# Kernel optimization log

Measured on AMD Instinct MI355X. Metric: run time of the kernel, lower is better.

Reference implementation:

```python
import jax, jax.numpy as jnp
import numpy as np

N_ENT = 14951   # entities (FB15K-style multimodal KG)
N_REL = 1345    # relations == number of context sub-graphs
N_NODES = 120000  # nodes in the batched context graph (b_x length)
N_EDGES = 480000  # edges in the normalized batched adjacency


def _glorot(key, shape):
    scale = np.sqrt(2.0 / (shape[0] + shape[1])).astype(np.float32)
    return jax.random.normal(key, shape, dtype=jnp.float32) * scale


def setup_inputs() -> dict:
    key = jax.random.key(0)
    ks = jax.random.split(key, 16)
    inp = {}
    inp["img_feat"] = jax.random.normal(ks[0], (N_ENT, 4096), dtype=jnp.float32)
    inp["text_feat"] = jax.random.normal(ks[1], (N_ENT, 300), dtype=jnp.float32)
    inp["rel_emb"] = jax.random.normal(ks[2], (N_REL, 300), dtype=jnp.float32)
    # learned parameters (eval mode: dropout = identity)
    inp["W_img_text"] = _glorot(ks[3], (4396, 100)); inp["b_img_text"] = jnp.zeros((100,), jnp.float32)
    inp["W_rel_input"] = _glorot(ks[4], (300, 100)); inp["b_rel_input"] = jnp.zeros((100,), jnp.float32)
    inp["W_gc1"] = _glorot(ks[5], (200, 256)); inp["b_gc1"] = jnp.zeros((256,), jnp.float32)
    inp["W_gc2"] = _glorot(ks[6], (256, 200)); inp["b_gc2"] = jnp.zeros((200,), jnp.float32)
    inp["W_emb"] = _glorot(ks[7], (400, 1)); inp["b_emb"] = jnp.zeros((1,), jnp.float32)
    inp["W_emb_out"] = _glorot(ks[8], (400, 200)); inp["b_emb_out"] = jnp.zeros((200,), jnp.float32)
    inp["W_rel"] = _glorot(ks[9], (300, 200)); inp["b_rel"] = jnp.zeros((200,), jnp.float32)
    # row-normalized adjacency of the batched context graph, as edge list
    inp["edge_weight"] = jax.random.uniform(ks[10], (N_EDGES,), dtype=jnp.float32)
    inp["b_x"] = jax.random.randint(ks[11], (N_NODES,), 0, N_ENT)
    inp["b_graph"] = jax.random.randint(ks[12], (N_NODES,), 0, N_REL)
    inp["edge_src"] = jax.random.randint(ks[13], (N_EDGES,), 0, N_NODES)
    inp["edge_dst"] = jax.random.randint(ks[14], (N_EDGES,), 0, N_NODES)
    return inp


def reference(img_feat, text_feat, rel_emb, W_img_text, b_img_text, W_rel_input,
              b_rel_input, W_gc1, b_gc1, W_gc2, b_gc2, W_emb, b_emb, W_emb_out,
              b_emb_out, W_rel, b_rel, edge_weight, b_x, b_graph, edge_src, edge_dst):
    seg_sum = lambda v, idx, n: jax.ops.segment_sum(v, idx, num_segments=n)

    def spmm(h):  # normalized adjacency @ h via edge-list gather/scatter
        return seg_sum(h[edge_src] * edge_weight[:, None], edge_dst, N_NODES)

    # multimodal entity encoder: Linear(4396 -> 100)
    emf = jnp.concatenate([img_feat, text_feat], axis=1) @ W_img_text + b_img_text
    # relation context encoder: Linear(300 -> 100) + ReLU
    rel_in = jax.nn.relu(rel_emb @ W_rel_input + b_rel_input)
    # batched context-graph node features [M, 200]
    h = jnp.concatenate([emf[b_x], rel_in[b_graph]], axis=1)
    # two-layer GCN encoder (SGCN1)
    h1 = jax.nn.relu(spmm(h @ W_gc1) + b_gc1)
    h2 = spmm(h1 @ W_gc2) + b_gc2          # [M, 200]
    # scatter_mean over entity ids, broadcast back
    cnt = seg_sum(jnp.ones((N_NODES,), h2.dtype), b_x, N_ENT)
    mean = seg_sum(h2, b_x, N_ENT) / jnp.maximum(cnt, 1.0)[:, None]
    emb = jnp.concatenate([h2, mean[b_x]], axis=1)   # [M, 400]
    score = emb @ W_emb + b_emb                      # [M, 1]
    # scatter_softmax over segments b_x (numerically stable)
    smax = jax.ops.segment_max(score, b_x, num_segments=N_ENT)
    e = jnp.exp(score - smax[b_x])
    z_s = e / seg_sum(e, b_x, N_ENT)[b_x]
    new_out = seg_sum(z_s * emb, b_x, N_ENT) @ W_emb_out + b_emb_out  # [N_ENT, 200]
    # relation output encoder: Linear(300 -> 200) + ReLU
    rel_context = jax.nn.relu(rel_emb @ W_rel + b_rel)                # [N_REL, 200]
    return new_out, rel_context
```

## Files before the change

### kernel.cpp

```cpp
#include <hip/hip_runtime.h>

#define N_ENT 14951
#define N_REL 1345
#define NNODE 120000
#define NEDGE 480000
#define MP_ENC 14976
#define KP_ENC 4608
#define NP_ENC 112
#define ENC_SPLIT 16
#define ENC_KSPLIT 288
#define ENC_STEPS 9
#define MROWS1 16320
#define NB_E 118
#define NB_N 15

static inline int ceil_div(int a, int b){ return (a + b - 1) / b; }

typedef __bf16 bf16x8 __attribute__((ext_vector_type(8)));
typedef float f32x4 __attribute__((ext_vector_type(4)));

__device__ inline unsigned short f2bf(float f){
  unsigned u = __float_as_uint(f);
  return (unsigned short)((u + 0x7fffu + ((u >> 16) & 1u)) >> 16);
}
__device__ inline float bf2f(unsigned short b){
  return __uint_as_float(((unsigned)b) << 16);
}

__global__ __launch_bounds__(256) void enc_mfma(
    const float* __restrict__ img, const float* __restrict__ txt,
    const unsigned short* __restrict__ Wt1, float* __restrict__ part)
{
  __shared__ unsigned short As[64 * 40];
  __shared__ unsigned short Bs[112 * 40];
  const int t = threadIdx.x;
  const int m0 = blockIdx.x * 64;
  const int s = blockIdx.y;
  const int l = t & 63, w = t >> 6;
  f32x4 acc[7];
  #pragma unroll
  for (int i = 0; i < 7; i++) acc[i] = f32x4{0.f, 0.f, 0.f, 0.f};

  for (int step = 0; step < ENC_STEPS; ++step) {
    const int kb = s * ENC_KSPLIT + step * 32;
    #pragma unroll
    for (int p = 0; p < 2; ++p) {
      const int c = t + p * 256;
      const int row = c >> 3, kq = c & 7;
      const int rowg = m0 + row;
      const int k = kb + kq * 4;
      float4 v = make_float4(0.f, 0.f, 0.f, 0.f);
      if (rowg < N_ENT) {
        if (k < 4096)      v = *(const float4*)(img + (size_t)rowg * 4096 + k);
        else if (k < 4396) v = *(const float4*)(txt + (size_t)rowg * 300 + (k - 4096));
      }
      ushort4 b;
      b.x = f2bf(v.x); b.y = f2bf(v.y); b.z = f2bf(v.z); b.w = f2bf(v.w);
      *(ushort4*)&As[row * 40 + kq * 4] = b;
    }
    {
      const int n = t >> 2, k16 = t & 3;
      *(uint4*)&Bs[n * 40 + k16 * 8] = *(const uint4*)(Wt1 + (size_t)n * KP_ENC + kb + k16 * 8);
      if (t < 192) {
        const int c = t + 256;
        const int n2 = c >> 2, k2 = c & 3;
        *(uint4*)&Bs[n2 * 40 + k2 * 8] = *(const uint4*)(Wt1 + (size_t)n2 * KP_ENC + kb + k2 * 8);
      }
    }
    __syncthreads();
    bf16x8 a = *(const bf16x8*)&As[(w * 16 + (l & 15)) * 40 + (l >> 4) * 8];
    #pragma unroll
    for (int ct = 0; ct < 7; ++ct) {
      bf16x8 bb = *(const bf16x8*)&Bs[(ct * 16 + (l & 15)) * 40 + (l >> 4) * 8];
      acc[ct] = __builtin_amdgcn_mfma_f32_16x16x32_bf16(a, bb, acc[ct], 0, 0, 0);
    }
    __syncthreads();
  }
  const int rb = m0 + w * 16 + (l >> 4) * 4;
  const int col = l & 15;
  float* pp = part + (size_t)s * MP_ENC * NP_ENC;
  #pragma unroll
  for (int ct = 0; ct < 7; ++ct)
    #pragma unroll
    for (int i = 0; i < 4; ++i)
      pp[(size_t)(rb + i) * NP_ENC + ct * 16 + col] = acc[ct][i];
}

__global__ __launch_bounds__(256) void enc_reduce(
    const float* __restrict__ part, const float* __restrict__ bias,
    unsigned short* __restrict__ feat1)
{
  int i = blockIdx.x * 256 + threadIdx.x;
  if (i >= N_ENT * 100) return;
  int r = i / 100, c = i % 100;
  float v = bias[c];
  #pragma unroll
  for (int s = 0; s < ENC_SPLIT; ++s) v += part[((size_t)s * MP_ENC + r) * NP_ENC + c];
  feat1[(size_t)r * 224 + c] = f2bf(v);
}

__global__ __launch_bounds__(256) void rin_pack(
    const float* __restrict__ rin, unsigned short* __restrict__ feat1)
{
  int i = blockIdx.x * 256 + threadIdx.x;
  if (i >= N_REL * 100) return;
  int r = i / 100, c = i % 100;
  feat1[(size_t)(N_ENT + r) * 224 + 100 + c] = f2bf(rin[i]);
}

__global__ __launch_bounds__(256) void egr1_mfma(
    const unsigned short* __restrict__ feat1, const unsigned short* __restrict__ Wtg1,
    unsigned short* __restrict__ egr1)
{
  __shared__ unsigned short As[64 * 40];
  __shared__ unsigned short Bs[256 * 40];
  const int t = threadIdx.x;
  const int m0 = blockIdx.x * 64;
  const int l = t & 63, w = t >> 6;
  f32x4 acc[16];
  #pragma unroll
  for (int i = 0; i < 16; i++) acc[i] = f32x4{0.f, 0.f, 0.f, 0.f};

  for (int step = 0; step < 7; ++step) {
    const int kb = step * 32;
    {
      const int row = t >> 2, kc = t & 3;
      *(uint4*)&As[row * 40 + kc * 8] = *(const uint4*)(feat1 + (size_t)(m0 + row) * 224 + kb + kc * 8);
    }
    #pragma unroll
    for (int p = 0; p < 4; ++p) {
      const int c = t + p * 256;
      const int n = c >> 2, k16 = c & 3;
      *(uint4*)&Bs[n * 40 + k16 * 8] = *(const uint4*)(Wtg1 + (size_t)n * 224 + kb + k16 * 8);
    }
    __syncthreads();
    bf16x8 a = *(const bf16x8*)&As[(w * 16 + (l & 15)) * 40 + (l >> 4) * 8];
    #pragma unroll
    for (int ct = 0; ct < 16; ++ct) {
      bf16x8 bb = *(const bf16x8*)&Bs[(ct * 16 + (l & 15)) * 40 + (l >> 4) * 8];
      acc[ct] = __builtin_amdgcn_mfma_f32_16x16x32_bf16(a, bb, acc[ct], 0, 0, 0);
    }
    __syncthreads();
  }
  const int rb = m0 + w * 16 + (l >> 4) * 4;
  const int col0 = l & 15;
  #pragma unroll
  for (int ct = 0; ct < 16; ++ct) {
    const int col = ct * 16 + col0;
    #pragma unroll
    for (int i = 0; i < 4; ++i)
      egr1[(size_t)(rb + i) * 256 + col] = f2bf(acc[ct][i]);
  }
}

__global__ __launch_bounds__(256) void gemm2_mfma(
    const unsigned short* __restrict__ h1, const unsigned short* __restrict__ Wt2,
    unsigned short* __restrict__ hg2)
{
  __shared__ unsigned short As[64 * 40];
  __shared__ unsigned short Bs[208 * 40];
  const int t = threadIdx.x;
  const int m0 = blockIdx.x * 64;
  const int l = t & 63, w = t >> 6;
  f32x4 acc[13];
  #pragma unroll
  for (int i = 0; i < 13; i++) acc[i] = f32x4{0.f, 0.f, 0.f, 0.f};

  for (int step = 0; step < 8; ++step) {
    const int kb = step * 32;
    {
      const int row = t >> 2, kc = t & 3;
      *(uint4*)&As[row * 40 + kc * 8] = *(const uint4*)(h1 + (size_t)(m0 + row) * 256 + kb + kc * 8);
    }
    #pragma unroll
    for (int p = 0; p < 4; ++p) {
      const int c = t + p * 256;
      if (c < 832) {
        const int n = c >> 2, k16 = c & 3;
        *(uint4*)&Bs[n * 40 + k16 * 8] = *(const uint4*)(Wt2 + (size_t)n * 256 + kb + k16 * 8);
      }
    }
    __syncthreads();
    bf16x8 a = *(const bf16x8*)&As[(w * 16 + (l & 15)) * 40 + (l >> 4) * 8];
    #pragma unroll
    for (int ct = 0; ct < 13; ++ct) {
      bf16x8 bb = *(const bf16x8*)&Bs[(ct * 16 + (l & 15)) * 40 + (l >> 4) * 8];
      acc[ct] = __builtin_amdgcn_mfma_f32_16x16x32_bf16(a, bb, acc[ct], 0, 0, 0);
    }
    __syncthreads();
  }
  const int rb = m0 + w * 16 + (l >> 4) * 4;
  const int col0 = l & 15;
  #pragma unroll
  for (int ct = 0; ct < 13; ++ct) {
    const int col = ct * 16 + col0;
    #pragma unroll
    for (int i = 0; i < 4; ++i)
      hg2[(size_t)(rb + i) * 208 + col] = f2bf(acc[ct][i]);
  }
}

__global__ __launch_bounds__(256) void fin_mfma(
    const unsigned short* __restrict__ embA, const unsigned short* __restrict__ Wteo,
    const float* __restrict__ b_eo, float* __restrict__ out)
{
  __shared__ unsigned short As[64 * 40];
  __shared__ unsigned short Bs[208 * 40];
  const int t = threadIdx.x;
  const int m0 = blockIdx.x * 64;
  const int l = t & 63, w = t >> 6;
  f32x4 acc[13];
  #pragma unroll
  for (int i = 0; i < 13; i++) acc[i] = f32x4{0.f, 0.f, 0.f, 0.f};

  for (int step = 0; step < 13; ++step) {
    const int kb = step * 32;
    {
      const int row = t >> 2, kc = t & 3;
      *(uint4*)&As[row * 40 + kc * 8] = *(const uint4*)(embA + (size_t)(m0 + row) * 416 + kb + kc * 8);
    }
    #pragma unroll
    for (int p = 0; p < 4; ++p) {
      const int c = t + p * 256;
      if (c < 832) {
        const int n = c >> 2, k16 = c & 3;
        *(uint4*)&Bs[n * 40 + k16 * 8] = *(const uint4*)(Wteo + (size_t)n * 416 + kb + k16 * 8);
      }
    }
    __syncthreads();
    bf16x8 a = *(const bf16x8*)&As[(w * 16 + (l & 15)) * 40 + (l >> 4) * 8];
    #pragma unroll
    for (int ct = 0; ct < 13; ++ct) {
      bf16x8 bb = *(const bf16x8*)&Bs[(ct * 16 + (l & 15)) * 40 + (l >> 4) * 8];
      acc[ct] = __builtin_amdgcn_mfma_f32_16x16x32_bf16(a, bb, acc[ct], 0, 0, 0);
    }
    __syncthreads();
  }
  const int rb = m0 + w * 16 + (l >> 4) * 4;
  const int col0 = l & 15;
  #pragma unroll
  for (int ct = 0; ct < 13; ++ct) {
    const int col = ct * 16 + col0;
    if (col < 200) {
      const float b = b_eo[col];
      #pragma unroll
      for (int i = 0; i < 4; ++i) {
        const int r = rb + i;
        if (r < N_ENT) out[(size_t)r * 200 + col] = acc[ct][i] + b;
      }
    }
  }
}

__global__ __launch_bounds__(256) void wt_all_k(
    const float* __restrict__ W_it, const float* __restrict__ W_g1,
    const float* __restrict__ W_g2, const float* __restrict__ W_eo,
    unsigned short* __restrict__ Wt1, unsigned short* __restrict__ Wtg1,
    unsigned short* __restrict__ Wt2, unsigned short* __restrict__ Wteo)
{
  int i = blockIdx.x * 256 + threadIdx.x;
  if (i < NP_ENC * KP_ENC) {
    int n = i / KP_ENC, k = i % KP_ENC;
    float v = (n < 100 && k < 4396) ? W_it[(size_t)k * 100 + n] : 0.f;
    Wt1[i] = f2bf(v);
    return;
  }
  i -= NP_ENC * KP_ENC;
  if (i < 256 * 224) {
    int n = i / 224, k = i % 224;
    float v = (k < 200) ? W_g1[(size_t)k * 256 + n] : 0.f;
    Wtg1[i] = f2bf(v);
    return;
  }
  i -= 256 * 224;
  if (i < 208 * 256) {
    int n = i >> 8, k = i & 255;
    float v = (n < 200) ? W_g2[(size_t)k * 200 + n] : 0.f;
    Wt2[i] = f2bf(v);
    return;
  }
  i -= 208 * 256;
  if (i < 208 * 416) {
    int n = i / 416, k = i % 416;
    float v = (n < 200 && k < 400) ? W_eo[(size_t)k * 200 + n] : 0.f;
    Wteo[i] = f2bf(v);
  }
}

template<bool RELU, bool HASBIAS>
__global__ __launch_bounds__(256) void gemm_f32(
    const float* __restrict__ A1, int K1, const float* __restrict__ A2,
    const float* __restrict__ B, const float* __restrict__ bias,
    float* __restrict__ C, int M, int K, int N)
{
  constexpr int BM = 64, BN = 128, BK = 16;
  __shared__ float As[BK][BM + 4];
  __shared__ float Bs[BK][BN];
  const int t = threadIdx.x;
  const int m0 = blockIdx.y * BM, n0 = blockIdx.x * BN;
  const int tr = t >> 4, tc = t & 15;
  const int tm0 = tr * 4, tn0 = tc * 8;
  const int K2 = K - K1;
  const int arow = t >> 2, aq = (t & 3) * 4;
  const int brow = t >> 4, bc0 = (t & 15) * 4;
  float acc[4][8];
  #pragma unroll
  for (int i = 0; i < 4; i++)
    #pragma unroll
    for (int j = 0; j < 8; j++) acc[i][j] = 0.f;

  for (int k0 = 0; k0 < K; k0 += BK) {
    {
      const int r = m0 + arow;
      const int k = k0 + aq;
      float4 v = make_float4(0.f, 0.f, 0.f, 0.f);
      if (r < M) {
        if (k + 3 < K1) {
          v = *(const float4*)(A1 + (size_t)r * K1 + k);
        } else if (k >= K1 && (k - K1) + 3 < K2) {
          v = *(const float4*)(A2 + (size_t)r * K2 + (k - K1));
        } else {
          float tmp[4] = {0.f, 0.f, 0.f, 0.f};
          #pragma unroll
          for (int j = 0; j < 4; j++) {
            int kj = k + j;
            if (kj < K) tmp[j] = (kj < K1) ? A1[(size_t)r * K1 + kj]
                                           : A2[(size_t)r * K2 + (kj - K1)];
          }
          v = make_float4(tmp[0], tmp[1], tmp[2], tmp[3]);
        }
      }
      As[aq + 0][arow] = v.x; As[aq + 1][arow] = v.y;
      As[aq + 2][arow] = v.z; As[aq + 3][arow] = v.w;
    }
    {
      const int k = k0 + brow;
      #pragma unroll
      for (int h = 0; h < 2; h++) {
        const int n = n0 + bc0 + h * 64;
        float4 v = make_float4(0.f, 0.f, 0.f, 0.f);
        if (k < K) {
          if (n + 3 < N) {
            v = *(const float4*)(B + (size_t)k * N + n);
          } else {
            float tmp[4] = {0.f, 0.f, 0.f, 0.f};
            for (int j = 0; j < 4; j++) if (n + j < N) tmp[j] = B[(size_t)k * N + n + j];
            v = make_float4(tmp[0], tmp[1], tmp[2], tmp[3]);
          }
        }
        *(float4*)&Bs[brow][bc0 + h * 64] = v;
      }
    }
    __syncthreads();
    #pragma unroll
    for (int k = 0; k < BK; k++) {
      float a[4], b[8];
      *(float4*)&a[0] = *(const float4*)&As[k][tm0];
      *(float4*)&b[0] = *(const float4*)&Bs[k][tn0];
      *(float4*)&b[4] = *(const float4*)&Bs[k][tn0 + 4];
      #pragma unroll
      for (int i = 0; i < 4; i++)
        #pragma unroll
        for (int j = 0; j < 8; j++) acc[i][j] = fmaf(a[i], b[j], acc[i][j]);
    }
    __syncthreads();
  }
  #pragma unroll
  for (int i = 0; i < 4; i++) {
    const int r = m0 + tm0 + i;
    if (r >= M) continue;
    #pragma unroll
    for (int j = 0; j < 8; j++) {
      const int c = n0 + tn0 + j;
      if (c >= N) continue;
      float v = acc[i][j];
      if (HASBIAS) v += bias[c];
      if (RELU) v = fmaxf(v, 0.f);
      C[(size_t)r * N + c] = v;
    }
  }
}

__global__ __launch_bounds__(256) void hist2_k(
    const int* __restrict__ edst, const int* __restrict__ bx,
    int* __restrict__ ehist, int* __restrict__ nhist)
{
  int i = blockIdx.x * 256 + threadIdx.x;
  if (i < NEDGE) { atomicAdd(&ehist[edst[i]], 1); return; }
  i -= NEDGE;
  if (i < NNODE) atomicAdd(&nhist[bx[i]], 1);
}

__global__ __launch_bounds__(256) void scan1_k(
    const int* __restrict__ ehist, int* __restrict__ ebase, int* __restrict__ epart,
    const int* __restrict__ nhist, int* __restrict__ nbase, int* __restrict__ npart)
{
  __shared__ int s[256];
  const int t = threadIdx.x;
  const bool eregion = blockIdx.x < NB_E;
  const int b = eregion ? blockIdx.x : blockIdx.x - NB_E;
  const int n = eregion ? NNODE : N_ENT;
  const int* hist = eregion ? ehist : nhist;
  int* base = eregion ? ebase : nbase;
  int* partial = eregion ? epart : npart;
  const int i0 = b * 1024 + t * 4;
  int v[4];
  #pragma unroll
  for (int j = 0; j < 4; j++) v[j] = (i0 + j < n) ? hist[i0 + j] : 0;
  const int tsum = v[0] + v[1] + v[2] + v[3];
  s[t] = tsum;
  __syncthreads();
  #pragma unroll
  for (int off = 1; off < 256; off <<= 1) {
    int u = (t >= off) ? s[t - off] : 0;
    __syncthreads();
    s[t] += u;
    __syncthreads();
  }
  int run = s[t] - tsum;
  #pragma unroll
  for (int j = 0; j < 4; j++) {
    if (i0 + j < n) base[i0 + j] = run;
    run += v[j];
  }
  if (t == 255) partial[b] = s[255];
}

__global__ __launch_bounds__(256) void scan2_k(
    int* __restrict__ epart, int* __restrict__ ebase_end,
    int* __restrict__ npart, int* __restrict__ nbase_end)
{
  __shared__ int s[256];
  const int t = threadIdx.x;
  const bool eregion = blockIdx.x == 0;
  int* partial = eregion ? epart : npart;
  const int nb = eregion ? NB_E : NB_N;
  const int v = (t < nb) ? partial[t] : 0;
  s[t] = v;
  __syncthreads();
  #pragma unroll
  for (int off = 1; off < 256; off <<= 1) {
    int u = (t >= off) ? s[t - off] : 0;
    __syncthreads();
    s[t] += u;
    __syncthreads();
  }
  if (t < nb) partial[t] = s[t] - v;
  if (t == 255) *(eregion ? ebase_end : nbase_end) = s[255];
}

#define NB3_E 469
__global__ __launch_bounds__(256) void scan3_k(
    int* __restrict__ ebase, const int* __restrict__ epart,
    int* __restrict__ nbase, const int* __restrict__ npart)
{
  if (blockIdx.x < NB3_E) {
    int i = blockIdx.x * 256 + threadIdx.x;
    if (i < NNODE) ebase[i] += epart[i >> 10];
  } else {
    int i = (blockIdx.x - NB3_E) * 256 + threadIdx.x;
    if (i < N_ENT) nbase[i] += npart[i >> 10];
  }
}

__global__ __launch_bounds__(256) void scatter2_k(
    const int* __restrict__ esrc, const int* __restrict__ edst, const float* __restrict__ ew,
    const int* __restrict__ bx, const int* __restrict__ bg,
    const int* __restrict__ ebase, int* __restrict__ ecur,
    float* __restrict__ s_w, int* __restrict__ s_src,
    int* __restrict__ s_en, int* __restrict__ s_gn,
    const int* __restrict__ nbase, int* __restrict__ ncur, int* __restrict__ node_of)
{
  int i = blockIdx.x * 256 + threadIdx.x;
  if (i < NEDGE) {
    int d = edst[i];
    int p = ebase[d] + atomicAdd(&ecur[d], 1);
    int s = esrc[i];
    s_w[p] = ew[i];
    s_src[p] = s;
    s_en[p] = bx[s];
    s_gn[p] = bg[s];
    return;
  }
  i -= NEDGE;
  if (i < NNODE) {
    int ent = bx[i];
    int p = nbase[ent] + atomicAdd(&ncur[ent], 1);
    node_of[p] = i;
  }
}

__global__ __launch_bounds__(256) void spmm1_g(
    const int* __restrict__ ebase, const float* __restrict__ s_w,
    const int* __restrict__ s_en, const int* __restrict__ s_gn,
    const unsigned short* __restrict__ egr1,
    const float* __restrict__ b_g1, unsigned short* __restrict__ h1)
{
  const int gid = blockIdx.x * blockDim.x + threadIdx.x;
  const int d = gid >> 6, lane = gid & 63;
  if (d >= NNODE) return;
  const int p0 = ebase[d], p1 = ebase[d + 1];
  float acc[4] = {0.f, 0.f, 0.f, 0.f};
  for (int p = p0; p < p1; ++p) {
    const float w = s_w[p];
    const int en = s_en[p], gn = s_gn[p];
    const ushort4 va = *(const ushort4*)(egr1 + (size_t)en * 256 + lane * 4);
    const ushort4 vb = *(const ushort4*)(egr1 + (size_t)(N_ENT + gn) * 256 + lane * 4);
    acc[0] += w * (bf2f(va.x) + bf2f(vb.x));
    acc[1] += w * (bf2f(va.y) + bf2f(vb.y));
    acc[2] += w * (bf2f(va.z) + bf2f(vb.z));
    acc[3] += w * (bf2f(va.w) + bf2f(vb.w));
  }
  const float4 b = ((const float4*)b_g1)[lane];
  ushort4 o;
  o.x = f2bf(fmaxf(acc[0] + b.x, 0.f));
  o.y = f2bf(fmaxf(acc[1] + b.y, 0.f));
  o.z = f2bf(fmaxf(acc[2] + b.z, 0.f));
  o.w = f2bf(fmaxf(acc[3] + b.w, 0.f));
  *(ushort4*)(h1 + (size_t)d * 256 + lane * 4) = o;
}

__global__ __launch_bounds__(256) void spmm2_g(
    const int* __restrict__ ebase, const float* __restrict__ s_w,
    const int* __restrict__ s_src, const unsigned short* __restrict__ hg2,
    const float* __restrict__ b_g2, const float* __restrict__ W_e,
    unsigned short* __restrict__ h2, float* __restrict__ score)
{
  const int gid = blockIdx.x * blockDim.x + threadIdx.x;
  const int d = gid >> 6, lane = gid & 63;
  if (d >= NNODE) return;
  const int p0 = ebase[d], p1 = ebase[d + 1];
  float acc[4] = {0.f, 0.f, 0.f, 0.f};
  const int col = lane * 4;
  float sp = 0.f;
  if (lane < 50) {
    for (int p = p0; p < p1; ++p) {
      const float w = s_w[p];
      const ushort4 v = *(const ushort4*)(hg2 + (size_t)s_src[p] * 208 + col);
      acc[0] += w * bf2f(v.x); acc[1] += w * bf2f(v.y);
      acc[2] += w * bf2f(v.z); acc[3] += w * bf2f(v.w);
    }
    const float4 b = ((const float4*)b_g2)[lane];
    acc[0] += b.x; acc[1] += b.y; acc[2] += b.z; acc[3] += b.w;
    ushort4 o;
    o.x = f2bf(acc[0]); o.y = f2bf(acc[1]); o.z = f2bf(acc[2]); o.w = f2bf(acc[3]);
    *(ushort4*)(h2 + (size_t)d * 200 + col) = o;
    const float4 we = ((const float4*)W_e)[lane];
    sp = acc[0] * we.x + acc[1] * we.y + acc[2] * we.z + acc[3] * we.w;
  }
  #pragma unroll
  for (int off = 32; off; off >>= 1) sp += __shfl_xor(sp, off);
  if (lane == 0) score[d] = sp;
}

__global__ __launch_bounds__(256) void ent_k(
    const int* __restrict__ nbase, const int* __restrict__ node_of,
    const unsigned short* __restrict__ h2, const float* __restrict__ score,
    unsigned short* __restrict__ embA)
{
  const int gid = blockIdx.x * blockDim.x + threadIdx.x;
  const int ent = gid >> 6, lane = gid & 63;
  if (ent >= N_ENT) return;
  const int p0 = nbase[ent], p1 = nbase[ent + 1];
  const int cnt = p1 - p0;
  float m = -3.4e38f;
  for (int p = p0 + lane; p < p1; p += 64) m = fmaxf(m, score[node_of[p]]);
  #pragma unroll
  for (int off = 32; off; off >>= 1) m = fmaxf(m, __shfl_xor(m, off));
  float es = 0.f;
  for (int p = p0 + lane; p < p1; p += 64) es += __expf(score[node_of[p]] - m);
  #pragma unroll
  for (int off = 32; off; off >>= 1) es += __shfl_xor(es, off);
  const float inv_es = (cnt > 0) ? 1.f / es : 0.f;
  const float inv_cnt = 1.f / fmaxf((float)cnt, 1.f);
  float aw[4] = {0.f, 0.f, 0.f, 0.f};
  float am[4] = {0.f, 0.f, 0.f, 0.f};
  for (int p = p0; p < p1; ++p) {
    const int nd = node_of[p];
    const float z = __expf(score[nd] - m) * inv_es;
    if (lane < 50) {
      const ushort4 v = *(const ushort4*)(h2 + (size_t)nd * 200 + lane * 4);
      const float vx = bf2f(v.x), vy = bf2f(v.y), vz = bf2f(v.z), vw = bf2f(v.w);
      aw[0] += z * vx; aw[1] += z * vy; aw[2] += z * vz; aw[3] += z * vw;
      am[0] += vx; am[1] += vy; am[2] += vz; am[3] += vw;
    }
  }
  if (lane < 50) {
    ushort4 ow, om;
    ow.x = f2bf(aw[0]); ow.y = f2bf(aw[1]); ow.z = f2bf(aw[2]); ow.w = f2bf(aw[3]);
    om.x = f2bf(am[0] * inv_cnt); om.y = f2bf(am[1] * inv_cnt);
    om.z = f2bf(am[2] * inv_cnt); om.w = f2bf(am[3] * inv_cnt);
    *(ushort4*)(embA + (size_t)ent * 416 + lane * 4) = ow;
    *(ushort4*)(embA + (size_t)ent * 416 + 200 + lane * 4) = om;
  }
}

extern "C" void kernel_launch(void* const* d_in, const int* in_sizes, int n_in,
                              void* d_out, int out_size, void* d_ws, size_t ws_size,
                              hipStream_t stream)
{
  const float* img  = (const float*)d_in[0];
  const float* txt  = (const float*)d_in[1];
  const float* rel  = (const float*)d_in[2];
  const float* W_it = (const float*)d_in[3];
  const float* b_it = (const float*)d_in[4];
  const float* W_ri = (const float*)d_in[5];
  const float* b_ri = (const float*)d_in[6];
  const float* W_g1 = (const float*)d_in[7];
  const float* b_g1 = (const float*)d_in[8];
  const float* W_g2 = (const float*)d_in[9];
  const float* b_g2 = (const float*)d_in[10];
  const float* W_e  = (const float*)d_in[11];
  const float* W_eo = (const float*)d_in[13];
  const float* b_eo = (const float*)d_in[14];
  const float* W_r  = (const float*)d_in[15];
  const float* b_r  = (const float*)d_in[16];
  const float* ew   = (const float*)d_in[17];
  const int*   bx   = (const int*)d_in[18];
  const int*   bg   = (const int*)d_in[19];
  const int*   esrc = (const int*)d_in[20];
  const int*   edst = (const int*)d_in[21];

  float* ws = (float*)d_ws;
  size_t off = 0;
  auto alloc = [&](size_t n){ size_t r = off; off += (n + 255) & ~(size_t)255; return r; };
  unsigned short* feat1 = (unsigned short*)(ws + alloc((size_t)MROWS1 * 224 / 2));
  unsigned short* egr1  = (unsigned short*)(ws + alloc((size_t)MROWS1 * 256 / 2));
  unsigned short* h1    = (unsigned short*)(ws + alloc((size_t)NNODE * 256 / 2));
  unsigned short* hg2   = (unsigned short*)(ws + alloc((size_t)NNODE * 208 / 2));
  unsigned short* embA  = (unsigned short*)(ws + alloc((size_t)MP_ENC * 416 / 2));
  unsigned short* h2    = (unsigned short*)(ws + alloc((size_t)NNODE * 200 / 2));
  float* part  = ws + alloc((size_t)ENC_SPLIT * MP_ENC * NP_ENC);
  float* rin   = ws + alloc((size_t)N_REL * 100);
  float* score = ws + alloc(NNODE);
  size_t cnt0 = alloc((size_t)NNODE * 2 + (size_t)N_ENT * 2);
  int* ehist = (int*)(ws + cnt0);
  int* ecur  = ehist + NNODE;
  int* nhist = ecur + NNODE;
  int* ncur  = nhist + N_ENT;
  int* ebase = (int*)(ws + alloc(NNODE + 1));
  int* nbase = (int*)(ws + alloc(N_ENT + 1));
  int* epart = (int*)(ws + alloc(256));
  int* npart = (int*)(ws + alloc(256));
  float* s_w  = ws + alloc(NEDGE);
  int* s_src  = (int*)(ws + alloc(NEDGE));
  int* s_en   = (int*)(ws + alloc(NEDGE));
  int* s_gn   = (int*)(ws + alloc(NEDGE));
  int* node_of = (int*)(ws + alloc(NNODE));
  unsigned short* Wt1  = (unsigned short*)(ws + alloc((size_t)NP_ENC * KP_ENC / 2));
  unsigned short* Wtg1 = (unsigned short*)(ws + alloc((size_t)256 * 224 / 2));
  unsigned short* Wt2  = (unsigned short*)(ws + alloc((size_t)208 * 256 / 2));
  unsigned short* Wteo = (unsigned short*)(ws + alloc((size_t)208 * 416 / 2));

  dim3 blk(256);

  hipMemsetAsync(ehist, 0, ((size_t)NNODE * 2 + (size_t)N_ENT * 2) * 4, stream);
  hipMemsetAsync(feat1, 0, (size_t)MROWS1 * 224 * 2, stream);
  hipMemsetAsync(embA,  0, (size_t)MP_ENC * 416 * 2, stream);

  hist2_k<<<ceil_div(NEDGE + NNODE, 256), blk, 0, stream>>>(edst, bx, ehist, nhist);
  scan1_k<<<NB_E + NB_N, blk, 0, stream>>>(ehist, ebase, epart, nhist, nbase, npart);
  scan2_k<<<2, blk, 0, stream>>>(epart, ebase + NNODE, npart, nbase + N_ENT);
  scan3_k<<<NB3_E + ceil_div(N_ENT, 256), blk, 0, stream>>>(ebase, epart, nbase, npart);
  scatter2_k<<<ceil_div(NEDGE + NNODE, 256), blk, 0, stream>>>(
      esrc, edst, ew, bx, bg, ebase, ecur, s_w, s_src, s_en, s_gn, nbase, ncur, node_of);

  wt_all_k<<<ceil_div(NP_ENC * KP_ENC + 256 * 224 + 208 * 256 + 208 * 416, 256), blk, 0, stream>>>(
      W_it, W_g1, W_g2, W_eo, Wt1, Wtg1, Wt2, Wteo);

  enc_mfma<<<dim3(MP_ENC / 64, ENC_SPLIT), blk, 0, stream>>>(img, txt, Wt1, part);
  enc_reduce<<<ceil_div(N_ENT * 100, 256), blk, 0, stream>>>(part, b_it, feat1);
  gemm_f32<true, true><<<dim3(1, ceil_div(N_REL, 64)), blk, 0, stream>>>(
      rel, 300, rel, W_ri, b_ri, rin, N_REL, 300, 100);
  rin_pack<<<ceil_div(N_REL * 100, 256), blk, 0, stream>>>(rin, feat1);

  egr1_mfma<<<MROWS1 / 64, blk, 0, stream>>>(feat1, Wtg1, egr1);
  spmm1_g<<<ceil_div(NNODE * 64, 256), blk, 0, stream>>>(
      ebase, s_w, s_en, s_gn, egr1, b_g1, h1);

  gemm2_mfma<<<NNODE / 64, blk, 0, stream>>>(h1, Wt2, hg2);
  spmm2_g<<<ceil_div(NNODE * 64, 256), blk, 0, stream>>>(
      ebase, s_w, s_src, hg2, b_g2, W_e, h2, score);

  ent_k<<<ceil_div(N_ENT * 64, 256), blk, 0, stream>>>(nbase, node_of, h2, score, embA);

  float* out_new = (float*)d_out;
  float* out_rel = out_new + (size_t)N_ENT * 200;
  fin_mfma<<<MP_ENC / 64, blk, 0, stream>>>(embA, Wteo, b_eo, out_new);
  gemm_f32<true, true><<<dim3(2, ceil_div(N_REL, 64)), blk, 0, stream>>>(
      rel, 300, rel, W_r, b_r, out_rel, N_REL, 300, 200);
}
```

Measured before the change: 629.0 us.

## Cut encoder K-split, fuse relation encoder, fast path for small entity segments

The image/text encoder GEMM drops its split-K factor from 16 to 4 and trims the padded K from 4608 to 4480, cutting partial-sum traffic and the work of enc_reduce at the cost of fewer blocks in flight. The relation input encoder GEMM and its bf16 pack kernel are merged into one per-relation kernel that writes ReLU'd bf16 values straight into feat1. ent_k gains a single-pass path for entities with at most 64 nodes, reading each score once instead of twice.

```diff
diff --git a/kernel.cpp b/kernel.cpp
--- a/kernel.cpp
+++ b/kernel.cpp
@@ -5,11 +5,11 @@
 #define NNODE 120000
 #define NEDGE 480000
 #define MP_ENC 14976
-#define KP_ENC 4608
+#define KP_ENC 4480
 #define NP_ENC 112
-#define ENC_SPLIT 16
-#define ENC_KSPLIT 288
-#define ENC_STEPS 9
+#define ENC_SPLIT 4
+#define ENC_KSPLIT 1120
+#define ENC_STEPS 35
 #define MROWS1 16320
 #define NB_E 118
 #define NB_N 15
@@ -99,13 +99,22 @@
   feat1[(size_t)r * 224 + c] = f2bf(v);
 }
 
-__global__ __launch_bounds__(256) void rin_pack(
-    const float* __restrict__ rin, unsigned short* __restrict__ feat1)
-{
-  int i = blockIdx.x * 256 + threadIdx.x;
-  if (i >= N_REL * 100) return;
-  int r = i / 100, c = i % 100;
-  feat1[(size_t)(N_ENT + r) * 224 + 100 + c] = f2bf(rin[i]);
+__global__ __launch_bounds__(256) void rel_enc(
+    const float* __restrict__ rel, const float* __restrict__ W_ri,
+    const float* __restrict__ b_ri, unsigned short* __restrict__ feat1)
+{
+  __shared__ float rs[300];
+  const int r = blockIdx.x;
+  const int t = threadIdx.x;
+  if (t < 75) {
+    float4 v = *(const float4*)(rel + (size_t)r * 300 + t * 4);
+    *(float4*)&rs[t * 4] = v;
+  }
+  __syncthreads();
+  if (t >= 100) return;
+  float s = b_ri[t];
+  for (int k = 0; k < 300; ++k) s = fmaf(rs[k], W_ri[(size_t)k * 100 + t], s);
+  feat1[(size_t)(N_ENT + r) * 224 + 100 + t] = f2bf(fmaxf(s, 0.f));
 }
 
 __global__ __launch_bounds__(256) void egr1_mfma(
@@ -563,14 +572,26 @@
   if (ent >= N_ENT) return;
   const int p0 = nbase[ent], p1 = nbase[ent + 1];
   const int cnt = p1 - p0;
-  float m = -3.4e38f;
-  for (int p = p0 + lane; p < p1; p += 64) m = fmaxf(m, score[node_of[p]]);
-  #pragma unroll
-  for (int off = 32; off; off >>= 1) m = fmaxf(m, __shfl_xor(m, off));
-  float es = 0.f;
-  for (int p = p0 + lane; p < p1; p += 64) es += __expf(score[node_of[p]] - m);
-  #pragma unroll
-  for (int off = 32; off; off >>= 1) es += __shfl_xor(es, off);
+  float m, es;
+  if (cnt <= 64) {
+    float sc = -3.4e38f;
+    if (p0 + lane < p1) sc = score[node_of[p0 + lane]];
+    m = sc;
+    #pragma unroll
+    for (int off = 32; off; off >>= 1) m = fmaxf(m, __shfl_xor(m, off));
+    es = (p0 + lane < p1) ? __expf(sc - m) : 0.f;
+    #pragma unroll
+    for (int off = 32; off; off >>= 1) es += __shfl_xor(es, off);
+  } else {
+    m = -3.4e38f;
+    for (int p = p0 + lane; p < p1; p += 64) m = fmaxf(m, score[node_of[p]]);
+    #pragma unroll
+    for (int off = 32; off; off >>= 1) m = fmaxf(m, __shfl_xor(m, off));
+    es = 0.f;
+    for (int p = p0 + lane; p < p1; p += 64) es += __expf(score[node_of[p]] - m);
+    #pragma unroll
+    for (int off = 32; off; off >>= 1) es += __shfl_xor(es, off);
+  }
   const float inv_es = (cnt > 0) ? 1.f / es : 0.f;
   const float inv_cnt = 1.f / fmaxf((float)cnt, 1.f);
   float aw[4] = {0.f, 0.f, 0.f, 0.f};
@@ -631,7 +652,6 @@
   unsigned short* embA  = (unsigned short*)(ws + alloc((size_t)MP_ENC * 416 / 2));
   unsigned short* h2    = (unsigned short*)(ws + alloc((size_t)NNODE * 200 / 2));
   float* part  = ws + alloc((size_t)ENC_SPLIT * MP_ENC * NP_ENC);
-  float* rin   = ws + alloc((size_t)N_REL * 100);
   float* score = ws + alloc(NNODE);
   size_t cnt0 = alloc((size_t)NNODE * 2 + (size_t)N_ENT * 2);
   int* ehist = (int*)(ws + cnt0);
@@ -670,9 +690,7 @@
 
   enc_mfma<<<dim3(MP_ENC / 64, ENC_SPLIT), blk, 0, stream>>>(img, txt, Wt1, part);
   enc_reduce<<<ceil_div(N_ENT * 100, 256), blk, 0, stream>>>(part, b_it, feat1);
-  gemm_f32<true, true><<<dim3(1, ceil_div(N_REL, 64)), blk, 0, stream>>>(
-      rel, 300, rel, W_ri, b_ri, rin, N_REL, 300, 100);
-  rin_pack<<<ceil_div(N_REL * 100, 256), blk, 0, stream>>>(rin, feat1);
+  rel_enc<<<N_REL, blk, 0, stream>>>(rel, W_ri, b_ri, feat1);
 
   egr1_mfma<<<MROWS1 / 64, blk, 0, stream>>>(feat1, Wtg1, egr1);
   spmm1_g<<<ceil_div(NNODE * 64, 256), blk, 0, stream>>>(
```

Result: faster. 567.8 us (-9.7%).
